# Kernel optimization log

Measured on AMD Instinct MI355X. Metric: run time of the kernel, lower is better.

The kernel has to match this reference:

```python
import jax, jax.numpy as jnp
import numpy as np

D, H, FF, E, K, B, S = 1024, 16, 4096, 8, 2, 2, 2048
EPS = 1e-5


def _layernorm(x, g, b):
    mu = x.mean(-1, keepdims=True)
    var = x.var(-1, keepdims=True)
    return (x - mu) * jax.lax.rsqrt(var + EPS) * g + b


def setup_inputs() -> dict:
    key = jax.random.key(0)
    ks = jax.random.split(key, 16)
    s = 0.02
    return {
        "x": jax.random.normal(ks[0], (B, S, D), dtype=jnp.float32),
        "in_proj_w": jax.random.normal(ks[1], (3 * D, D), dtype=jnp.float32) * s,
        "in_proj_b": jnp.zeros((3 * D,), jnp.float32),
        "out_proj_w": jax.random.normal(ks[2], (D, D), dtype=jnp.float32) * s,
        "out_proj_b": jnp.zeros((D,), jnp.float32),
        "ln1_g": jnp.ones((D,), jnp.float32),
        "ln1_b": jnp.zeros((D,), jnp.float32),
        "ln2_g": jnp.ones((D,), jnp.float32),
        "ln2_b": jnp.zeros((D,), jnp.float32),
        "gate_w": jax.random.normal(ks[3], (E, D), dtype=jnp.float32) * s,
        "gate_b": jnp.zeros((E,), jnp.float32),
        "w1": jax.random.normal(ks[4], (E, FF, D), dtype=jnp.float32) * s,
        "b1": jnp.zeros((E, FF), jnp.float32),
        "w2": jax.random.normal(ks[5], (E, D, FF), dtype=jnp.float32) * s,
        "b2": jnp.zeros((E, D), jnp.float32),
    }


def reference(x, in_proj_w, in_proj_b, out_proj_w, out_proj_b,
              ln1_g, ln1_b, ln2_g, ln2_b,
              gate_w, gate_b, w1, b1, w2, b2):
    b, s, d = x.shape
    hd = d // H
    # --- self-attention (pre-LN), dropout = identity (eval) ---
    normed = _layernorm(x, ln1_g, ln1_b)
    qkv = normed @ in_proj_w.T + in_proj_b            # [b,s,3d]
    q, k, v = jnp.split(qkv, 3, axis=-1)
    q = q.reshape(b, s, H, hd).transpose(0, 2, 1, 3)  # [b,h,s,hd]
    k = k.reshape(b, s, H, hd).transpose(0, 2, 1, 3)
    v = v.reshape(b, s, H, hd).transpose(0, 2, 1, 3)
    scores = jnp.einsum('bhqe,bhke->bhqk', q, k) / np.sqrt(hd)
    attn = jax.nn.softmax(scores, axis=-1)
    o = jnp.einsum('bhqk,bhke->bhqe', attn, v)
    o = o.transpose(0, 2, 1, 3).reshape(b, s, d)
    attn_out = o @ out_proj_w.T + out_proj_b
    x = x + attn_out
    present_kv = (normed, normed)
    # --- MoE FFN ---
    n2 = _layernorm(x, ln2_g, ln2_b)
    xf = n2.reshape(-1, d)                             # [T,d]
    T = xf.shape[0]
    logits = xf @ gate_w.T + gate_b                    # [T,E]
    probs = jax.nn.softmax(logits, axis=-1)
    top_v, top_i = jax.lax.top_k(probs, K)             # [T,K]
    top_v = top_v / top_v.sum(-1, keepdims=True)
    # combine weights per (token, expert); topk indices are unique per token
    cw = jnp.zeros((T, E), probs.dtype).at[jnp.arange(T)[:, None], top_i].add(top_v)
    # dense all-experts FFN (mathematically identical to masked gather/scatter)
    h = jnp.einsum('td,efd->etf', xf, w1) + b1[:, None, :]   # [E,T,FF]
    h = jax.nn.gelu(h, approximate=False)
    eo = jnp.einsum('etf,edf->etd', h, w2) + b2[:, None, :]  # [E,T,d]
    moe_out = jnp.einsum('te,etd->td', cw, eo)               # [T,d]
    out = x + moe_out.reshape(b, s, d)
    # --- load balance loss (Switch) ---
    top1 = jnp.argmax(probs, axis=-1)
    f = jnp.mean(jax.nn.one_hot(top1, E, dtype=probs.dtype), axis=0)
    P = probs.mean(axis=0)
    load_loss = 0.01 * E * jnp.sum(f * P)
    return out, load_loss, probs.reshape(b, s, E), present_kv[0]
```

## Files before the change

### kernel.cpp

```cpp
#include <hip/hip_runtime.h>
#include <math.h>

#define D_ 1024
#define H_ 16
#define HD_ 64
#define FF_ 4096
#define E_ 8
#define B_ 2
#define S_ 2048
#define T_ 4096
#define MAXROWS 9216
#define MAXTILES 72

typedef unsigned short u16;
typedef __attribute__((ext_vector_type(4))) float f32x4;
typedef __attribute__((ext_vector_type(8))) __bf16 bf16x8;
typedef __attribute__((ext_vector_type(8))) _Float16 f16x8;
typedef __attribute__((ext_vector_type(4))) unsigned short u16x4;

__device__ __forceinline__ u16 f2bf(float f){
  union { float f; unsigned u; } v; v.f = f;
  unsigned r = v.u + 0x7fffu + ((v.u >> 16) & 1u);
  return (u16)(r >> 16);
}
__device__ __forceinline__ float bf2f(u16 h){
  union { unsigned u; float f; } v; v.u = ((unsigned)h) << 16;
  return v.f;
}
__device__ __forceinline__ void glds16(const void* g, void* l){
  __builtin_amdgcn_global_load_lds((const __attribute__((address_space(1))) void*)g,
                                   (__attribute__((address_space(3))) void*)l, 16, 0, 0);
}
__device__ __forceinline__ bf16x8 ld8(const u16* p){
  return *reinterpret_cast<const bf16x8*>(p);
}
__device__ __forceinline__ f16x8 ldH8(const _Float16* p){
  return *reinterpret_cast<const f16x8*>(p);
}
__device__ __forceinline__ f32x4 mfma16(bf16x8 a, bf16x8 b, f32x4 c){
  return __builtin_amdgcn_mfma_f32_16x16x32_bf16(a, b, c, 0, 0, 0);
}
__device__ __forceinline__ f32x4 mfmaH(f16x8 a, f16x8 b, f32x4 c){
  return __builtin_amdgcn_mfma_f32_16x16x32_f16(a, b, c, 0, 0, 0);
}
__device__ __forceinline__ unsigned pk16(float a, float b){
  auto pk = __builtin_amdgcn_cvt_pkrtz(a, b);
  return __builtin_bit_cast(unsigned, pk);
}

__global__ void __launch_bounds__(256) split_hl_kernel(const float* __restrict__ in, u16* __restrict__ hi,
                                                       u16* __restrict__ lo, int n4){
  int i = blockIdx.x*blockDim.x + threadIdx.x;
  if (i >= n4) return;
  float4 v = reinterpret_cast<const float4*>(in)[i];
  float vv[4] = {v.x, v.y, v.z, v.w};
  u16x4 h, l;
  #pragma unroll
  for (int j=0;j<4;j++){
    u16 hh = f2bf(vv[j]);
    h[j] = hh;
    l[j] = f2bf(vv[j] - bf2f(hh));
  }
  reinterpret_cast<u16x4*>(hi)[i] = h;
  reinterpret_cast<u16x4*>(lo)[i] = l;
}

__global__ void __launch_bounds__(256) cvt_bf_kernel(const float* __restrict__ in, u16* __restrict__ out, int n4){
  int i = blockIdx.x*blockDim.x + threadIdx.x;
  if (i >= n4) return;
  float4 v = reinterpret_cast<const float4*>(in)[i];
  u16x4 o;
  o[0]=f2bf(v.x); o[1]=f2bf(v.y); o[2]=f2bf(v.z); o[3]=f2bf(v.w);
  reinterpret_cast<u16x4*>(out)[i] = o;
}

__global__ void __launch_bounds__(256) cvt_f16_kernel(const float* __restrict__ in, _Float16* __restrict__ out, int n4){
  int i = blockIdx.x*blockDim.x + threadIdx.x;
  if (i >= n4) return;
  float4 v = reinterpret_cast<const float4*>(in)[i];
  union { unsigned w[2]; u16x4 u; } o;
  o.w[0] = pk16(v.x, v.y);
  o.w[1] = pk16(v.z, v.w);
  reinterpret_cast<u16x4*>(out)[i] = o.u;
}

template<int OUTMODE>
__global__ void __launch_bounds__(256) ln_kernel(const float* __restrict__ x, const float* __restrict__ g,
    const float* __restrict__ bta, float* __restrict__ outf, u16* __restrict__ nout)
{
  const int t = blockIdx.x, tid = threadIdx.x;
  const float4 v = reinterpret_cast<const float4*>(x + (size_t)t*D_)[tid];
  float s  = v.x+v.y+v.z+v.w;
  float s2 = v.x*v.x+v.y*v.y+v.z*v.z+v.w*v.w;
  #pragma unroll
  for (int o=32;o;o>>=1){ s += __shfl_xor(s,o); s2 += __shfl_xor(s2,o); }
  __shared__ float rs[4], rq[4];
  const int wid=tid>>6, lane=tid&63;
  if (lane==0){ rs[wid]=s; rq[wid]=s2; }
  __syncthreads();
  s  = rs[0]+rs[1]+rs[2]+rs[3];
  s2 = rq[0]+rq[1]+rq[2]+rq[3];
  const float mu  = s*(1.0f/D_);
  const float var = s2*(1.0f/D_) - mu*mu;
  const float inv = rsqrtf(var + 1e-5f);
  const float4 gv = reinterpret_cast<const float4*>(g)[tid];
  const float4 bv = reinterpret_cast<const float4*>(bta)[tid];
  float oo[4];
  oo[0] = (v.x-mu)*inv*gv.x + bv.x;
  oo[1] = (v.y-mu)*inv*gv.y + bv.y;
  oo[2] = (v.z-mu)*inv*gv.z + bv.z;
  oo[3] = (v.w-mu)*inv*gv.w + bv.w;
  const size_t base = (size_t)t*D_ + tid*4;
  if (outf){ outf[base]=oo[0]; outf[base+1]=oo[1]; outf[base+2]=oo[2]; outf[base+3]=oo[3]; }
  if (OUTMODE==1){
    union { unsigned w[2]; u16x4 u; } hv;
    hv.w[0] = pk16(oo[0], oo[1]);
    hv.w[1] = pk16(oo[2], oo[3]);
    reinterpret_cast<u16x4*>(nout)[base>>2] = hv.u;
  } else {
    u16x4 hv;
    hv[0]=f2bf(oo[0]); hv[1]=f2bf(oo[1]); hv[2]=f2bf(oo[2]); hv[3]=f2bf(oo[3]);
    reinterpret_cast<u16x4*>(nout)[base>>2] = hv;
  }
}

__global__ void __launch_bounds__(256) qkv_kernel(
    const _Float16* __restrict__ A, const _Float16* __restrict__ Bw,
    const float* __restrict__ bias,
    _Float16* __restrict__ qf, _Float16* __restrict__ kf, _Float16* __restrict__ vtf)
{
  __shared__ __align__(16) _Float16 Ash[2][128*32], Bsh[2][128*32];
  const int bid = blockIdx.x, nwg = gridDim.x;
  const int fid = (bid & 7)*(nwg>>3) + (bid>>3);
  const int nt = fid % 24, mt = fid / 24;
  const int tid=threadIdx.x, wid=tid>>6, lane=tid&63;
  const int wr=wid>>1, wc=wid&1;
  const int r16=lane&15, g4=lane>>4;
  const _Float16* Ag = A  + (size_t)mt*128*D_;
  const _Float16* Bg = Bw + (size_t)nt*128*D_;
  const int srow = wid*16 + (lane>>2);
  const int scol = (((lane&3) ^ ((lane>>3)&3)))*8;
  const int sl   = (g4 ^ ((r16>>1)&3))*8;
  f32x4 acc[4][4] = {};
#define QSTAGE(bi, k0) do { \
    _Pragma("unroll") \
    for (int p=0;p<2;p++){ \
      const int r  = p*64 + srow; \
      const int lo = (p*64 + wid*16)*32; \
      glds16(Ag + (size_t)r*D_ + (k0) + scol, &Ash[bi][lo]); \
      glds16(Bg + (size_t)r*D_ + (k0) + scol, &Bsh[bi][lo]); \
    } \
  } while(0)
  QSTAGE(0, 0);
  int cur = 0;
  for (int t=0; t<D_/32; ++t){
    if (t+1 < D_/32){
      QSTAGE(cur^1, (t+1)*32);
      asm volatile("s_waitcnt vmcnt(4)" ::: "memory");
    } else {
      asm volatile("s_waitcnt vmcnt(0)" ::: "memory");
    }
    __syncthreads();
    f16x8 af[4], bfr[4];
    #pragma unroll
    for (int m=0;m<4;m++) af[m]=ldH8(&Ash[cur][(wr*64+m*16+r16)*32 + sl]);
    #pragma unroll
    for (int n=0;n<4;n++) bfr[n]=ldH8(&Bsh[cur][(wc*64+n*16+r16)*32 + sl]);
    #pragma unroll
    for (int m=0;m<4;m++){
      #pragma unroll
      for (int n=0;n<4;n++) acc[m][n] = mfmaH(af[m], bfr[n], acc[m][n]);
    }
    __syncthreads();
    cur ^= 1;
  }
#undef QSTAGE
  #pragma unroll
  for (int m=0;m<4;m++){
    #pragma unroll
    for (int n=0;n<4;n++){
      #pragma unroll
      for (int r=0;r<4;r++){
        const int grow = mt*128 + wr*64 + m*16 + g4*4 + r;
        const int gcol = nt*128 + wc*64 + n*16 + r16;
        const float val = acc[m][n][r] + bias[gcol];
        const int which = gcol>>10, rem = gcol&1023;
        const int hh = rem>>6, ee = rem&63;
        const int bb = grow>>11, ss = grow&2047;
        if (which==0){
          qf[((size_t)(bb*H_+hh)*S_ + ss)*HD_ + ee] = (_Float16)(val * 0.18033688f);
        } else if (which==1){
          kf[((size_t)(bb*H_+hh)*S_ + ss)*HD_ + ee] = (_Float16)val;
        } else {
          const int p32 = 2*(ss & 12) + (ss & 3) + 4*((ss >> 4) & 1);
          const size_t idx = (((size_t)(bb*H_+hh)*(S_/32) + (ss>>5))*HD_ + ee)*32 + p32;
          vtf[idx] = (_Float16)val;
        }
      }
    }
  }
}

__global__ void __launch_bounds__(256) gemm3_kernel(
    const u16* __restrict__ Ah, const u16* __restrict__ Al, int lda,
    const u16* __restrict__ Bh, const u16* __restrict__ Bl, int Kdim,
    const float* __restrict__ bias,
    const float* __restrict__ resid, float* __restrict__ x1out)
{
  __shared__ __align__(16) u16 Ash[2][128*32], Asl[2][128*32], Bsh[2][128*32], Bsl[2][128*32];
  const int bid = blockIdx.x, nwg = gridDim.x;
  const int fid = (bid & 7)*(nwg>>3) + (bid>>3);
  const int nt = fid & 7, mt = fid >> 3;
  const int tid=threadIdx.x, wid=tid>>6, lane=tid&63;
  const int wr=wid>>1, wc=wid&1;
  const int r16=lane&15, g4=lane>>4;
  const u16* Agh = Ah + (size_t)mt*128*lda;
  const u16* Agl = Al + (size_t)mt*128*lda;
  const u16* Bgh = Bh + (size_t)nt*128*Kdim;
  const u16* Bgl = Bl + (size_t)nt*128*Kdim;
  const int srow = wid*16 + (lane>>2);
  const int scol = (((lane&3) ^ ((lane>>3)&3)))*8;
  const int sl   = (g4 ^ ((r16>>1)&3))*8;
  f32x4 acc[4][4] = {};
#define G3STAGE(bi, k0) do { \
    _Pragma("unroll") \
    for (int p=0;p<2;p++){ \
      const int r  = p*64 + srow; \
      const int lo = (p*64 + wid*16)*32; \
      glds16(Agh + (size_t)r*lda  + (k0) + scol, &Ash[bi][lo]); \
      glds16(Agl + (size_t)r*lda  + (k0) + scol, &Asl[bi][lo]); \
      glds16(Bgh + (size_t)r*Kdim + (k0) + scol, &Bsh[bi][lo]); \
      glds16(Bgl + (size_t)r*Kdim + (k0) + scol, &Bsl[bi][lo]); \
    } \
  } while(0)
  G3STAGE(0, 0);
  int cur = 0;
  const int NK = Kdim/32;
  for (int t=0; t<NK; ++t){
    if (t+1 < NK){
      G3STAGE(cur^1, (t+1)*32);
      asm volatile("s_waitcnt vmcnt(8)" ::: "memory");
    } else {
      asm volatile("s_waitcnt vmcnt(0)" ::: "memory");
    }
    __syncthreads();
    bf16x8 afh[4], afl[4], bfh[4], bfl[4];
    #pragma unroll
    for (int m=0;m<4;m++){
      const int row = wr*64 + m*16 + r16;
      afh[m] = ld8(&Ash[cur][row*32 + sl]);
      afl[m] = ld8(&Asl[cur][row*32 + sl]);
    }
    #pragma unroll
    for (int n=0;n<4;n++){
      const int row = wc*64 + n*16 + r16;
      bfh[n] = ld8(&Bsh[cur][row*32 + sl]);
      bfl[n] = ld8(&Bsl[cur][row*32 + sl]);
    }
    #pragma unroll
    for (int m=0;m<4;m++){
      #pragma unroll
      for (int n=0;n<4;n++){
        acc[m][n] = mfma16(afl[m], bfh[n], acc[m][n]);
        acc[m][n] = mfma16(afh[m], bfl[n], acc[m][n]);
        acc[m][n] = mfma16(afh[m], bfh[n], acc[m][n]);
      }
    }
    __syncthreads();
    cur ^= 1;
  }
#undef G3STAGE
  #pragma unroll
  for (int m=0;m<4;m++){
    #pragma unroll
    for (int n=0;n<4;n++){
      #pragma unroll
      for (int r=0;r<4;r++){
        const int grow = mt*128 + wr*64 + m*16 + g4*4 + r;
        const int gcol = nt*128 + wc*64 + n*16 + r16;
        const float val = acc[m][n][r] + bias[gcol];
        const size_t idx = (size_t)grow*D_ + gcol;
        x1out[idx] = val + resid[idx];
      }
    }
  }
}

__global__ void __launch_bounds__(256) attn9_kernel(
    const _Float16* __restrict__ Qf, const _Float16* __restrict__ Kf,
    const _Float16* __restrict__ Vtf,
    u16* __restrict__ Oh, u16* __restrict__ Ol)
{
  __shared__ __align__(16) _Float16 Kb[2][4096];
  __shared__ __align__(16) _Float16 Vb[2][4096];
  const int bid = blockIdx.x;
  const int wg = (bid & 7) * 128 + (bid >> 3);
  const int bh = wg >> 5, qc = wg & 31;
  const int tid=threadIdx.x, wid=tid>>6, lane=tid&63;
  const int r16=lane&15, g4=lane>>4;
  const int q0 = qc*64 + wid*16;
  const _Float16* Qp = Qf  + (size_t)bh*S_*HD_ + (size_t)(q0+r16)*HD_ + g4*8;
  const _Float16* Kbase = Kf  + (size_t)bh*S_*HD_;
  const _Float16* Vbase = Vtf + (size_t)bh*HD_*S_;
  const f16x8 qf0 = ldH8(Qp);
  const f16x8 qf1 = ldH8(Qp+32);
  f32x4 of[4] = {};
  float m_run = -3e38f, lr = 0.f;

  const int kOff = (wid*8 + (lane>>3))*HD_ + (((lane&7) ^ ((lane>>3)&7)))*8;
  const int vOff = wid*512 + lane*8;
  const int sk0 = (g4 ^ (r16&7))*8;
  const int sk1 = ((g4+4) ^ (r16&7))*8;

#define STAGE(bi, tt) do { \
    glds16(Kbase + (size_t)(tt)*64*HD_ + kOff,          (void*)&Kb[bi][wid*512]); \
    glds16(Kbase + (size_t)(tt)*64*HD_ + 32*HD_ + kOff, (void*)&Kb[bi][2048 + wid*512]); \
    glds16(Vbase + (size_t)(tt)*4096 + vOff,            (void*)&Vb[bi][wid*512]); \
    glds16(Vbase + (size_t)(tt)*4096 + 2048 + vOff,     (void*)&Vb[bi][2048 + wid*512]); \
  } while(0)

#define ATT_HALF(Kh_, Vh_) do { \
    const f16x8 k0v = ldH8((Kh_) + r16*64 + sk0); \
    const f16x8 k1v = ldH8((Kh_) + r16*64 + sk1); \
    const f16x8 k2v = ldH8((Kh_) + (16+r16)*64 + sk0); \
    const f16x8 k3v = ldH8((Kh_) + (16+r16)*64 + sk1); \
    f32x4 sA={}, sB={}; \
    __builtin_amdgcn_s_setprio(1); \
    sA = mfmaH(k0v, qf0, sA); sA = mfmaH(k1v, qf1, sA); \
    sB = mfmaH(k2v, qf0, sB); sB = mfmaH(k3v, qf1, sB); \
    __builtin_amdgcn_s_setprio(0); \
    const float t0=sA[0], t1=sA[1], t2=sA[2], t3=sA[3]; \
    const float t4=sB[0], t5=sB[1], t6=sB[2], t7=sB[3]; \
    const float lmx = fmaxf(fmaxf(fmaxf(t0,t1),fmaxf(t2,t3)), \
                            fmaxf(fmaxf(t4,t5),fmaxf(t6,t7))); \
    if (!__all(lmx <= m_run + 4.0f)) { \
      float mx = fmaxf(lmx, __shfl_xor(lmx,16)); \
      mx = fmaxf(mx, __shfl_xor(mx,32)); \
      const float mn = fmaxf(m_run, mx); \
      const float alp = __builtin_amdgcn_exp2f(m_run - mn); \
      m_run = mn; \
      lr *= alp; \
      const float ao0=__shfl(alp,4*g4), ao1=__shfl(alp,4*g4+1); \
      const float ao2=__shfl(alp,4*g4+2), ao3=__shfl(alp,4*g4+3); \
      _Pragma("unroll") \
      for (int c=0;c<4;c++){ of[c][0]*=ao0; of[c][1]*=ao1; of[c][2]*=ao2; of[c][3]*=ao3; } \
    } \
    const float msh = m_run - 9.0f; \
    const float p0=__builtin_amdgcn_exp2f(t0-msh), p1=__builtin_amdgcn_exp2f(t1-msh); \
    const float p2=__builtin_amdgcn_exp2f(t2-msh), p3=__builtin_amdgcn_exp2f(t3-msh); \
    const float p4=__builtin_amdgcn_exp2f(t4-msh), p5=__builtin_amdgcn_exp2f(t5-msh); \
    const float p6=__builtin_amdgcn_exp2f(t6-msh), p7=__builtin_amdgcn_exp2f(t7-msh); \
    lr += ((p0+p1)+(p2+p3)) + ((p4+p5)+(p6+p7)); \
    union { unsigned w[4]; f16x8 v; } pu; \
    pu.w[0]=pk16(p0,p1); pu.w[1]=pk16(p2,p3); \
    pu.w[2]=pk16(p4,p5); pu.w[3]=pk16(p6,p7); \
    const f16x8 v0v = ldH8((Vh_) + (r16)*32 + g4*8); \
    const f16x8 v1v = ldH8((Vh_) + (16+r16)*32 + g4*8); \
    const f16x8 v2v = ldH8((Vh_) + (32+r16)*32 + g4*8); \
    const f16x8 v3v = ldH8((Vh_) + (48+r16)*32 + g4*8); \
    __builtin_amdgcn_s_setprio(1); \
    of[0] = mfmaH(pu.v, v0v, of[0]); of[1] = mfmaH(pu.v, v1v, of[1]); \
    of[2] = mfmaH(pu.v, v2v, of[2]); of[3] = mfmaH(pu.v, v3v, of[3]); \
    __builtin_amdgcn_s_setprio(0); \
  } while(0)

  STAGE(0, 0);
  int cur = 0;

  for (int t=0; t<32; ++t){
    if (t < 31){
      STAGE(cur^1, t+1);
      asm volatile("s_waitcnt vmcnt(4)" ::: "memory");
    } else {
      asm volatile("s_waitcnt vmcnt(0)" ::: "memory");
    }
    __syncthreads();
    ATT_HALF(&Kb[cur][0],    &Vb[cur][0]);
    ATT_HALF(&Kb[cur][2048], &Vb[cur][2048]);
    __syncthreads();
    cur ^= 1;
  }
#undef ATT_HALF
#undef STAGE

  lr += __shfl_xor(lr,16);
  lr += __shfl_xor(lr,32);
  float li[4];
  #pragma unroll
  for (int r=0;r<4;r++) li[r] = 1.0f / __shfl(lr, 4*g4+r);
  const int bb = bh>>4, hh = bh&15;
  #pragma unroll
  for (int c=0;c<4;c++){
    #pragma unroll
    for (int r=0;r<4;r++){
      const float val = of[c][r] * li[r];
      const int qq = q0 + 4*g4 + r;
      const size_t idx = ((size_t)(bb*S_+qq))*D_ + hh*HD_ + c*16 + r16;
      const u16 hi = f2bf(val);
      Oh[idx]=hi; Ol[idx]=f2bf(val-bf2f(hi));
    }
  }
}

__global__ void __launch_bounds__(64) gate_kernel(
    const float* __restrict__ x1, const float* __restrict__ g2, const float* __restrict__ b2v,
    const float* __restrict__ gw, const float* __restrict__ gb,
    float* __restrict__ probs_out, int* __restrict__ top_i, float* __restrict__ cw_w)
{
  const int t = blockIdx.x, lane = threadIdx.x;
  const float* row = x1 + (size_t)t*D_;
  float xv[16];
  float s=0.f, s2=0.f;
  #pragma unroll
  for (int j=0;j<4;j++){
    float4 v = reinterpret_cast<const float4*>(row)[lane*4+j];
    xv[j*4]=v.x; xv[j*4+1]=v.y; xv[j*4+2]=v.z; xv[j*4+3]=v.w;
    s += v.x+v.y+v.z+v.w; s2 += v.x*v.x+v.y*v.y+v.z*v.z+v.w*v.w;
  }
  #pragma unroll
  for (int o=32;o;o>>=1){ s+=__shfl_xor(s,o); s2+=__shfl_xor(s2,o); }
  const float mu=s*(1.f/D_), var=s2*(1.f/D_)-mu*mu, inv=rsqrtf(var+1e-5f);
  float nv[16];
  #pragma unroll
  for (int j=0;j<4;j++){
    float4 gv = reinterpret_cast<const float4*>(g2)[lane*4+j];
    float4 bv = reinterpret_cast<const float4*>(b2v)[lane*4+j];
    nv[j*4]  =(xv[j*4]  -mu)*inv*gv.x+bv.x;
    nv[j*4+1]=(xv[j*4+1]-mu)*inv*gv.y+bv.y;
    nv[j*4+2]=(xv[j*4+2]-mu)*inv*gv.z+bv.z;
    nv[j*4+3]=(xv[j*4+3]-mu)*inv*gv.w+bv.w;
  }
  float acc[E_] = {};
  #pragma unroll
  for (int e=0;e<E_;e++){
    const float* w = gw + (size_t)e*D_ + lane*16;
    #pragma unroll
    for (int j=0;j<4;j++){
      float4 wv = reinterpret_cast<const float4*>(w)[j];
      acc[e] += nv[j*4]*wv.x + nv[j*4+1]*wv.y + nv[j*4+2]*wv.z + nv[j*4+3]*wv.w;
    }
  }
  #pragma unroll
  for (int e=0;e<E_;e++){
    #pragma unroll
    for (int o=32;o;o>>=1) acc[e]+=__shfl_xor(acc[e],o);
  }
  float lg[E_], mx=-3e38f;
  #pragma unroll
  for (int e=0;e<E_;e++){ lg[e]=acc[e]+gb[e]; mx=fmaxf(mx,lg[e]); }
  float ex[E_], sm=0.f;
  #pragma unroll
  for (int e=0;e<E_;e++){ ex[e]=__expf(lg[e]-mx); sm+=ex[e]; }
  float p[E_];
  #pragma unroll
  for (int e=0;e<E_;e++) p[e]=ex[e]/sm;
  if (lane<E_) probs_out[(size_t)t*E_+lane]=p[lane];
  int i0=0; float l0=lg[0];
  #pragma unroll
  for (int e=1;e<E_;e++) if (lg[e]>l0){ l0=lg[e]; i0=e; }
  int i1=-1; float l1=-3e38f;
  #pragma unroll
  for (int e=0;e<E_;e++) if (e!=i0 && lg[e]>l1){ l1=lg[e]; i1=e; }
  if (lane==0){
    top_i[2*t]=i0; top_i[2*t+1]=i1;
    const float v0=p[i0], v1=p[i1];
    const float swt=v0+v1;
    cw_w[2*t]=v0/swt; cw_w[2*t+1]=v1/swt;
  }
}

__global__ void __launch_bounds__(512) scan_kernel(const int* __restrict__ top_i,
    int* __restrict__ goff, int* __restrict__ tile_expert,
    int* __restrict__ assign_token, int* __restrict__ pos_of)
{
  __shared__ int cnt[E_];
  __shared__ int off[E_+1];
  const int tid=threadIdx.x;
  if (tid<E_) cnt[tid]=0;
  __syncthreads();
  for (int t=tid;t<T_;t+=512){
    atomicAdd(&cnt[top_i[2*t]],1);
    atomicAdd(&cnt[top_i[2*t+1]],1);
  }
  __syncthreads();
  if (tid==0){
    off[0]=0;
    for (int e=0;e<E_;e++) off[e+1]=off[e]+((cnt[e]+127)&~127);
    for (int i=0;i<=E_;i++) goff[i]=off[i];
  }
  __syncthreads();
  if (tid<MAXTILES){
    const int r=tid*128; int e=-1;
    for (int j=0;j<E_;j++) if (r>=off[j] && r<off[j+1]) e=j;
    tile_expert[tid]=e;
  }
  const int lane=tid&63;
  const int e=tid>>6;
  int base=off[e];
  for (int c=0;c<T_/64;c++){
    const int t=c*64+lane;
    const int a0=top_i[2*t], a1=top_i[2*t+1];
    const bool f=(a0==e)||(a1==e);
    const unsigned long long m=__ballot(f);
    if (f){
      const int pos = base + (int)__popcll(m & ((1ull<<lane)-1ull));
      assign_token[pos]=t;
      pos_of[2*t + (a0==e?0:1)] = pos;
    }
    base += (int)__popcll(m);
  }
  for (int r=base+lane; r<off[e+1]; r+=64) assign_token[r]=-1;
  __syncthreads();
  for (int r=off[E_]+tid; r<MAXROWS; r+=512) assign_token[r]=-1;
}

__global__ void __launch_bounds__(256) gather_kernel(const int* __restrict__ assign_token,
    const u16* __restrict__ n2b, u16* __restrict__ xg)
{
  const int r = blockIdx.x;
  const int t = assign_token[r];
  u16x4 val = {};
  if (t>=0) val = reinterpret_cast<const u16x4*>(n2b + (size_t)t*D_)[threadIdx.x];
  reinterpret_cast<u16x4*>(xg + (size_t)r*D_)[threadIdx.x] = val;
}

template<int MODE>
__global__ void __launch_bounds__(256, 4) gemm_grp_kernel(
    const u16* __restrict__ A, int lda,
    const u16* __restrict__ Bbase, int Kdim, int Nsz, int NT,
    const float* __restrict__ bias,
    const int* __restrict__ tile_expert,
    u16* __restrict__ outp)
{
  const int bid = blockIdx.x, nwg = gridDim.x;
  const int fid = (bid & 7)*(nwg>>3) + (bid>>3);
  const int nt = fid % NT, mt = fid / NT;
  const int e = tile_expert[mt];
  if (e<0) return;
  __shared__ __align__(16) u16 Ash[2][128*32], Bsh[2][128*32];
  const int tid=threadIdx.x, wid=tid>>6, lane=tid&63;
  const int wr=wid>>1, wc=wid&1;
  const int r16=lane&15, g4=lane>>4;
  const u16* Ag = A + (size_t)mt*128*lda;
  const u16* Bg = Bbase + (size_t)e*Nsz*Kdim + (size_t)nt*128*Kdim;
  const float* bp = bias + (size_t)e*Nsz;
  const int srow = wid*16 + (lane>>2);
  const int scol = (((lane&3) ^ ((lane>>3)&3)))*8;
  const int sl   = (g4 ^ ((r16>>1)&3))*8;
  f32x4 acc[4][4] = {};
#define GSTAGE(bi, k0) do { \
    _Pragma("unroll") \
    for (int p=0;p<2;p++){ \
      const int r  = p*64+srow; \
      const int lo = (p*64+wid*16)*32; \
      glds16(Ag + (size_t)r*lda  + (k0) + scol, &Ash[bi][lo]); \
      glds16(Bg + (size_t)r*Kdim + (k0) + scol, &Bsh[bi][lo]); \
    } \
  } while(0)
  GSTAGE(0, 0);
  int cur = 0;
  const int NK = Kdim/32;
  for (int t=0; t<NK; ++t){
    if (t+1 < NK){
      GSTAGE(cur^1, (t+1)*32);
      asm volatile("s_waitcnt vmcnt(4)" ::: "memory");
    } else {
      asm volatile("s_waitcnt vmcnt(0)" ::: "memory");
    }
    __syncthreads();
    bf16x8 af[4], bfr[4];
    #pragma unroll
    for (int m=0;m<4;m++) af[m]=ld8(&Ash[cur][(wr*64+m*16+r16)*32 + sl]);
    #pragma unroll
    for (int n=0;n<4;n++) bfr[n]=ld8(&Bsh[cur][(wc*64+n*16+r16)*32 + sl]);
    #pragma unroll
    for (int m=0;m<4;m++){
      #pragma unroll
      for (int n=0;n<4;n++) acc[m][n] = mfma16(af[m], bfr[n], acc[m][n]);
    }
    __syncthreads();
    cur ^= 1;
  }
#undef GSTAGE
  #pragma unroll
  for (int m=0;m<4;m++){
    #pragma unroll
    for (int n=0;n<4;n++){
      #pragma unroll
      for (int r=0;r<4;r++){
        const int grow = mt*128 + wr*64 + m*16 + g4*4 + r;
        const int gcol = nt*128 + wc*64 + n*16 + r16;
        float val = acc[m][n][r] + bp[gcol];
        if (MODE==2){
          const float z = val*(1.0f + 0.044715f*val*val)*2.3021622f;
          val = val / (1.0f + __builtin_amdgcn_exp2f(-z));
        }
        outp[(size_t)grow*Nsz + gcol] = f2bf(val);
      }
    }
  }
}

__global__ void __launch_bounds__(256) combine_kernel(const float* __restrict__ x1,
    const u16* __restrict__ eo, const int* __restrict__ pos_of, const float* __restrict__ cw_w,
    float* __restrict__ out0)
{
  const int t=blockIdx.x, tid=threadIdx.x;
  const int r0=pos_of[2*t], r1=pos_of[2*t+1];
  const float w0=cw_w[2*t], w1=cw_w[2*t+1];
  const u16x4 e0 = reinterpret_cast<const u16x4*>(eo + (size_t)r0*D_)[tid];
  const u16x4 e1 = reinterpret_cast<const u16x4*>(eo + (size_t)r1*D_)[tid];
  const float4 xv = reinterpret_cast<const float4*>(x1 + (size_t)t*D_)[tid];
  float4 o;
  o.x = xv.x + w0*bf2f(e0[0]) + w1*bf2f(e1[0]);
  o.y = xv.y + w0*bf2f(e0[1]) + w1*bf2f(e1[1]);
  o.z = xv.z + w0*bf2f(e0[2]) + w1*bf2f(e1[2]);
  o.w = xv.w + w0*bf2f(e0[3]) + w1*bf2f(e1[3]);
  reinterpret_cast<float4*>(out0 + (size_t)t*D_)[tid] = o;
}

__global__ void __launch_bounds__(256) loss_kernel(const float* __restrict__ probs,
    const int* __restrict__ top_i, float* __restrict__ loss_out)
{
  const int tid=threadIdx.x;
  float f[E_]={0,0,0,0,0,0,0,0}, P[E_]={0,0,0,0,0,0,0,0};
  for (int t=tid;t<T_;t+=256){
    const float* pr = probs + (size_t)t*E_;
    const int a0 = top_i[2*t];
    #pragma unroll
    for (int e=0;e<E_;e++){
      P[e] += pr[e];
      f[e] += (a0==e) ? 1.0f : 0.0f;
    }
  }
  #pragma unroll
  for (int e=0;e<E_;e++){
    #pragma unroll
    for (int o=32;o;o>>=1){ f[e]+=__shfl_xor(f[e],o); P[e]+=__shfl_xor(P[e],o); }
  }
  __shared__ float sf[4][E_], sP[4][E_];
  const int wid=tid>>6, lane=tid&63;
  if (lane==0){
    #pragma unroll
    for (int e=0;e<E_;e++){ sf[wid][e]=f[e]; sP[wid][e]=P[e]; }
  }
  __syncthreads();
  if (tid==0){
    float loss=0.f;
    #pragma unroll
    for (int e=0;e<E_;e++){
      const float fe=sf[0][e]+sf[1][e]+sf[2][e]+sf[3][e];
      const float Pe=sP[0][e]+sP[1][e]+sP[2][e]+sP[3][e];
      loss += (fe/(float)T_)*(Pe/(float)T_);
    }
    loss_out[0] = 0.01f*(float)E_*loss;
  }
}

static inline size_t alup(size_t x){ return (x+255)&~(size_t)255; }

extern "C" void kernel_launch(void* const* d_in, const int* in_sizes, int n_in,
                              void* d_out, int out_size, void* d_ws, size_t ws_size,
                              hipStream_t stream) {
  (void)in_sizes; (void)n_in; (void)out_size; (void)ws_size;
  const float* x    = (const float*)d_in[0];
  const float* ipw  = (const float*)d_in[1];
  const float* ipb  = (const float*)d_in[2];
  const float* opw  = (const float*)d_in[3];
  const float* opb  = (const float*)d_in[4];
  const float* ln1g = (const float*)d_in[5];
  const float* ln1b = (const float*)d_in[6];
  const float* ln2g = (const float*)d_in[7];
  const float* ln2b = (const float*)d_in[8];
  const float* gw   = (const float*)d_in[9];
  const float* gb   = (const float*)d_in[10];
  const float* w1   = (const float*)d_in[11];
  const float* b1   = (const float*)d_in[12];
  const float* w2   = (const float*)d_in[13];
  const float* b2   = (const float*)d_in[14];

  float* out0       = (float*)d_out;
  float* loss_out   = out0 + (size_t)T_*D_;
  float* probs_out  = loss_out + 1;
  float* normed_out = probs_out + (size_t)T_*E_;

  char* p = (char*)d_ws;
  auto take = [&](size_t bytes)->void*{ void* r = (void*)p; p += alup(bytes); return r; };

  _Float16* wipf = (_Float16*)take((size_t)3*D_*D_*2);
  u16* wop_h = (u16*)take((size_t)D_*D_*2);
  u16* wop_l = (u16*)take((size_t)D_*D_*2);
  u16* w1b   = (u16*)take((size_t)E_*FF_*D_*2);
  u16* w2b   = (u16*)take((size_t)E_*D_*FF_*2);
  _Float16* nf16 = (_Float16*)take((size_t)T_*D_*2);
  _Float16* qf  = (_Float16*)take((size_t)T_*D_*2);
  _Float16* kf  = (_Float16*)take((size_t)T_*D_*2);
  _Float16* vtf = (_Float16*)take((size_t)T_*D_*2);
  u16* oh    = (u16*)take((size_t)T_*D_*2);
  u16* ol    = (u16*)take((size_t)T_*D_*2);
  float* x1  = (float*)take((size_t)T_*D_*4);
  u16* n2b   = (u16*)take((size_t)T_*D_*2);
  u16* xg    = (u16*)take((size_t)MAXROWS*D_*2);
  u16* hbuf  = (u16*)take((size_t)MAXROWS*FF_*2);
  u16* eo    = (u16*)take((size_t)MAXROWS*D_*2);
  int* top_i = (int*)take((size_t)T_*2*4);
  float* cww = (float*)take((size_t)T_*2*4);
  int* posof = (int*)take((size_t)T_*2*4);
  int* goff  = (int*)take((size_t)(E_+1)*4);
  int* texp  = (int*)take((size_t)MAXTILES*4);
  int* atok  = (int*)take((size_t)MAXROWS*4);

  cvt_f16_kernel<<<(3*D_*D_/4+255)/256, 256, 0, stream>>>(ipw, wipf, 3*D_*D_/4);
  split_hl_kernel<<<(D_*D_/4+255)/256, 256, 0, stream>>>(opw, wop_h, wop_l, D_*D_/4);
  cvt_bf_kernel<<<(E_*FF_*D_/4+255)/256, 256, 0, stream>>>(w1, w1b, E_*FF_*D_/4);
  cvt_bf_kernel<<<(E_*D_*FF_/4+255)/256, 256, 0, stream>>>(w2, w2b, E_*D_*FF_/4);

  ln_kernel<1><<<T_, 256, 0, stream>>>(x, ln1g, ln1b, normed_out, (u16*)nf16);

  qkv_kernel<<<dim3(24*(T_/128)), 256, 0, stream>>>(nf16, wipf, ipb, qf, kf, vtf);

  attn9_kernel<<<B_*H_*(S_/64), 256, 0, stream>>>(qf, kf, vtf, oh, ol);

  gemm3_kernel<<<dim3(8*(T_/128)), 256, 0, stream>>>(
      oh, ol, D_, wop_h, wop_l, D_, opb, x, x1);

  ln_kernel<2><<<T_, 256, 0, stream>>>(x1, ln2g, ln2b, nullptr, n2b);

  gate_kernel<<<T_, 64, 0, stream>>>(x1, ln2g, ln2b, gw, gb, probs_out, top_i, cww);

  scan_kernel<<<1, 512, 0, stream>>>(top_i, goff, texp, atok, posof);

  gather_kernel<<<MAXROWS, 256, 0, stream>>>(atok, n2b, xg);

  gemm_grp_kernel<2><<<dim3((FF_/128)*MAXTILES), 256, 0, stream>>>(xg, D_, w1b, D_, FF_, FF_/128, b1, texp, hbuf);
  gemm_grp_kernel<3><<<dim3((D_/128)*MAXTILES), 256, 0, stream>>>(hbuf, FF_, w2b, FF_, D_, D_/128, b2, texp, eo);

  combine_kernel<<<T_, 256, 0, stream>>>(x1, eo, posof, cww, out0);
  loss_kernel<<<1, 256, 0, stream>>>(probs_out, top_i, loss_out);
}
```

Measured before the change: 545.9 us.

## Convert expert weights to bf16 inside grouped GEMM and fuse gate into LN2

Drops the two standalone fp32-to-bf16 conversion kernels for the expert weights. The grouped GEMM now loads fp32 weight tiles into registers, converts them and writes them into swizzled LDS, with the global loads issued before the MFMAs and the LDS writes after them. Occupancy is lowered to 3 waves per SIMD. Separately, the router gate (logits, softmax, top-2) is fused into the second LayerNorm kernel so x1 is read once. The cost is more global bytes for the B operand per tile, repeated across token tiles, plus conversion ALU work inside the GEMM inner loop.

```diff
diff --git a/kernel.cpp b/kernel.cpp
--- a/kernel.cpp
+++ b/kernel.cpp
@@ -26,6 +26,9 @@
 __device__ __forceinline__ float bf2f(u16 h){
   union { unsigned u; float f; } v; v.u = ((unsigned)h) << 16;
   return v.f;
+}
+__device__ __forceinline__ unsigned pb2(float a, float b){
+  return (unsigned)f2bf(a) | ((unsigned)f2bf(b) << 16);
 }
 __device__ __forceinline__ void glds16(const void* g, void* l){
   __builtin_amdgcn_global_load_lds((const __attribute__((address_space(1))) void*)g,
@@ -65,15 +68,6 @@
   reinterpret_cast<u16x4*>(lo)[i] = l;
 }
 
-__global__ void __launch_bounds__(256) cvt_bf_kernel(const float* __restrict__ in, u16* __restrict__ out, int n4){
-  int i = blockIdx.x*blockDim.x + threadIdx.x;
-  if (i >= n4) return;
-  float4 v = reinterpret_cast<const float4*>(in)[i];
-  u16x4 o;
-  o[0]=f2bf(v.x); o[1]=f2bf(v.y); o[2]=f2bf(v.z); o[3]=f2bf(v.w);
-  reinterpret_cast<u16x4*>(out)[i] = o;
-}
-
 __global__ void __launch_bounds__(256) cvt_f16_kernel(const float* __restrict__ in, _Float16* __restrict__ out, int n4){
   int i = blockIdx.x*blockDim.x + threadIdx.x;
   if (i >= n4) return;
@@ -84,17 +78,20 @@
   reinterpret_cast<u16x4*>(out)[i] = o.u;
 }
 
-template<int OUTMODE>
+template<int OUTMODE, int GATE>
 __global__ void __launch_bounds__(256) ln_kernel(const float* __restrict__ x, const float* __restrict__ g,
-    const float* __restrict__ bta, float* __restrict__ outf, u16* __restrict__ nout)
+    const float* __restrict__ bta, float* __restrict__ outf, u16* __restrict__ nout,
+    const float* __restrict__ gw, const float* __restrict__ gb,
+    float* __restrict__ probs_out, int* __restrict__ top_i, float* __restrict__ cw_w)
 {
   const int t = blockIdx.x, tid = threadIdx.x;
+  __shared__ float rs[4], rq[4];
+  __shared__ float sp[4][E_];
   const float4 v = reinterpret_cast<const float4*>(x + (size_t)t*D_)[tid];
   float s  = v.x+v.y+v.z+v.w;
   float s2 = v.x*v.x+v.y*v.y+v.z*v.z+v.w*v.w;
   #pragma unroll
   for (int o=32;o;o>>=1){ s += __shfl_xor(s,o); s2 += __shfl_xor(s2,o); }
-  __shared__ float rs[4], rq[4];
   const int wid=tid>>6, lane=tid&63;
   if (lane==0){ rs[wid]=s; rq[wid]=s2; }
   __syncthreads();
@@ -121,6 +118,48 @@
     u16x4 hv;
     hv[0]=f2bf(oo[0]); hv[1]=f2bf(oo[1]); hv[2]=f2bf(oo[2]); hv[3]=f2bf(oo[3]);
     reinterpret_cast<u16x4*>(nout)[base>>2] = hv;
+  }
+  if (GATE){
+    float part[E_];
+    #pragma unroll
+    for (int e=0;e<E_;e++){
+      const float4 wv = reinterpret_cast<const float4*>(gw + (size_t)e*D_)[tid];
+      part[e] = oo[0]*wv.x + oo[1]*wv.y + oo[2]*wv.z + oo[3]*wv.w;
+    }
+    #pragma unroll
+    for (int e=0;e<E_;e++){
+      #pragma unroll
+      for (int o=32;o;o>>=1) part[e] += __shfl_xor(part[e], o);
+    }
+    if (lane==0){
+      #pragma unroll
+      for (int e=0;e<E_;e++) sp[wid][e] = part[e];
+    }
+    __syncthreads();
+    if (tid==0){
+      float lg[E_], mx=-3e38f;
+      #pragma unroll
+      for (int e=0;e<E_;e++){
+        lg[e] = sp[0][e]+sp[1][e]+sp[2][e]+sp[3][e] + gb[e];
+        mx = fmaxf(mx, lg[e]);
+      }
+      float ex[E_], sm=0.f;
+      #pragma unroll
+      for (int e=0;e<E_;e++){ ex[e]=__expf(lg[e]-mx); sm+=ex[e]; }
+      float p[E_];
+      #pragma unroll
+      for (int e=0;e<E_;e++){ p[e]=ex[e]/sm; probs_out[(size_t)t*E_+e]=p[e]; }
+      int i0=0; float l0=lg[0];
+      #pragma unroll
+      for (int e=1;e<E_;e++) if (lg[e]>l0){ l0=lg[e]; i0=e; }
+      int i1=-1; float l1=-3e38f;
+      #pragma unroll
+      for (int e=0;e<E_;e++) if (e!=i0 && lg[e]>l1){ l1=lg[e]; i1=e; }
+      top_i[2*t]=i0; top_i[2*t+1]=i1;
+      const float v0=p[i0], v1=p[i1];
+      const float swt=v0+v1;
+      cw_w[2*t]=v0/swt; cw_w[2*t+1]=v1/swt;
+    }
   }
 }
 
@@ -402,73 +441,6 @@
   }
 }
 
-__global__ void __launch_bounds__(64) gate_kernel(
-    const float* __restrict__ x1, const float* __restrict__ g2, const float* __restrict__ b2v,
-    const float* __restrict__ gw, const float* __restrict__ gb,
-    float* __restrict__ probs_out, int* __restrict__ top_i, float* __restrict__ cw_w)
-{
-  const int t = blockIdx.x, lane = threadIdx.x;
-  const float* row = x1 + (size_t)t*D_;
-  float xv[16];
-  float s=0.f, s2=0.f;
-  #pragma unroll
-  for (int j=0;j<4;j++){
-    float4 v = reinterpret_cast<const float4*>(row)[lane*4+j];
-    xv[j*4]=v.x; xv[j*4+1]=v.y; xv[j*4+2]=v.z; xv[j*4+3]=v.w;
-    s += v.x+v.y+v.z+v.w; s2 += v.x*v.x+v.y*v.y+v.z*v.z+v.w*v.w;
-  }
-  #pragma unroll
-  for (int o=32;o;o>>=1){ s+=__shfl_xor(s,o); s2+=__shfl_xor(s2,o); }
-  const float mu=s*(1.f/D_), var=s2*(1.f/D_)-mu*mu, inv=rsqrtf(var+1e-5f);
-  float nv[16];
-  #pragma unroll
-  for (int j=0;j<4;j++){
-    float4 gv = reinterpret_cast<const float4*>(g2)[lane*4+j];
-    float4 bv = reinterpret_cast<const float4*>(b2v)[lane*4+j];
-    nv[j*4]  =(xv[j*4]  -mu)*inv*gv.x+bv.x;
-    nv[j*4+1]=(xv[j*4+1]-mu)*inv*gv.y+bv.y;
-    nv[j*4+2]=(xv[j*4+2]-mu)*inv*gv.z+bv.z;
-    nv[j*4+3]=(xv[j*4+3]-mu)*inv*gv.w+bv.w;
-  }
-  float acc[E_] = {};
-  #pragma unroll
-  for (int e=0;e<E_;e++){
-    const float* w = gw + (size_t)e*D_ + lane*16;
-    #pragma unroll
-    for (int j=0;j<4;j++){
-      float4 wv = reinterpret_cast<const float4*>(w)[j];
-      acc[e] += nv[j*4]*wv.x + nv[j*4+1]*wv.y + nv[j*4+2]*wv.z + nv[j*4+3]*wv.w;
-    }
-  }
-  #pragma unroll
-  for (int e=0;e<E_;e++){
-    #pragma unroll
-    for (int o=32;o;o>>=1) acc[e]+=__shfl_xor(acc[e],o);
-  }
-  float lg[E_], mx=-3e38f;
-  #pragma unroll
-  for (int e=0;e<E_;e++){ lg[e]=acc[e]+gb[e]; mx=fmaxf(mx,lg[e]); }
-  float ex[E_], sm=0.f;
-  #pragma unroll
-  for (int e=0;e<E_;e++){ ex[e]=__expf(lg[e]-mx); sm+=ex[e]; }
-  float p[E_];
-  #pragma unroll
-  for (int e=0;e<E_;e++) p[e]=ex[e]/sm;
-  if (lane<E_) probs_out[(size_t)t*E_+lane]=p[lane];
-  int i0=0; float l0=lg[0];
-  #pragma unroll
-  for (int e=1;e<E_;e++) if (lg[e]>l0){ l0=lg[e]; i0=e; }
-  int i1=-1; float l1=-3e38f;
-  #pragma unroll
-  for (int e=0;e<E_;e++) if (e!=i0 && lg[e]>l1){ l1=lg[e]; i1=e; }
-  if (lane==0){
-    top_i[2*t]=i0; top_i[2*t+1]=i1;
-    const float v0=p[i0], v1=p[i1];
-    const float swt=v0+v1;
-    cw_w[2*t]=v0/swt; cw_w[2*t+1]=v1/swt;
-  }
-}
-
 __global__ void __launch_bounds__(512) scan_kernel(const int* __restrict__ top_i,
     int* __restrict__ goff, int* __restrict__ tile_expert,
     int* __restrict__ assign_token, int* __restrict__ pos_of)
@@ -525,9 +497,9 @@
 }
 
 template<int MODE>
-__global__ void __launch_bounds__(256, 4) gemm_grp_kernel(
+__global__ void __launch_bounds__(256, 3) gemm_grp_kernel(
     const u16* __restrict__ A, int lda,
-    const u16* __restrict__ Bbase, int Kdim, int Nsz, int NT,
+    const float* __restrict__ B32, int Kdim, int Nsz, int NT,
     const float* __restrict__ bias,
     const int* __restrict__ tile_expert,
     u16* __restrict__ outp)
@@ -541,33 +513,53 @@
   const int tid=threadIdx.x, wid=tid>>6, lane=tid&63;
   const int wr=wid>>1, wc=wid&1;
   const int r16=lane&15, g4=lane>>4;
-  const u16* Ag = A + (size_t)mt*128*lda;
-  const u16* Bg = Bbase + (size_t)e*Nsz*Kdim + (size_t)nt*128*Kdim;
+  const u16*   Ag   = A   + (size_t)mt*128*lda;
+  const float* Bg32 = B32 + (size_t)e*Nsz*Kdim + (size_t)nt*128*Kdim;
   const float* bp = bias + (size_t)e*Nsz;
   const int srow = wid*16 + (lane>>2);
   const int scol = (((lane&3) ^ ((lane>>3)&3)))*8;
   const int sl   = (g4 ^ ((r16>>1)&3))*8;
+  const int br = tid>>2, bg = tid&3;
+  const int bslot = (bg ^ ((br>>1)&3))*8;
+  float4 bv0, bv1, bv2, bv3;
   f32x4 acc[4][4] = {};
-#define GSTAGE(bi, k0) do { \
+#define ASTAGE(bi, k0) do { \
     _Pragma("unroll") \
     for (int p=0;p<2;p++){ \
       const int r  = p*64+srow; \
       const int lo = (p*64+wid*16)*32; \
-      glds16(Ag + (size_t)r*lda  + (k0) + scol, &Ash[bi][lo]); \
-      glds16(Bg + (size_t)r*Kdim + (k0) + scol, &Bsh[bi][lo]); \
+      glds16(Ag + (size_t)r*lda + (k0) + scol, &Ash[bi][lo]); \
     } \
   } while(0)
-  GSTAGE(0, 0);
+#define BLOAD(k0) do { \
+    const float* bp0 = Bg32 + (size_t)br*Kdim + (k0) + bg*8; \
+    const float* bp1 = Bg32 + (size_t)(br+64)*Kdim + (k0) + bg*8; \
+    bv0 = *reinterpret_cast<const float4*>(bp0); \
+    bv1 = *reinterpret_cast<const float4*>(bp0+4); \
+    bv2 = *reinterpret_cast<const float4*>(bp1); \
+    bv3 = *reinterpret_cast<const float4*>(bp1+4); \
+  } while(0)
+#define BWRITE(bi) do { \
+    uint4 w0, w1; \
+    w0.x = pb2(bv0.x,bv0.y); w0.y = pb2(bv0.z,bv0.w); \
+    w0.z = pb2(bv1.x,bv1.y); w0.w = pb2(bv1.z,bv1.w); \
+    w1.x = pb2(bv2.x,bv2.y); w1.y = pb2(bv2.z,bv2.w); \
+    w1.z = pb2(bv3.x,bv3.y); w1.w = pb2(bv3.z,bv3.w); \
+    *reinterpret_cast<uint4*>(&Bsh[bi][br*32 + bslot]) = w0; \
+    *reinterpret_cast<uint4*>(&Bsh[bi][(br+64)*32 + bslot]) = w1; \
+  } while(0)
+  BLOAD(0);
+  ASTAGE(0, 0);
+  BWRITE(0);
+  asm volatile("s_waitcnt vmcnt(0)" ::: "memory");
+  __syncthreads();
   int cur = 0;
   const int NK = Kdim/32;
   for (int t=0; t<NK; ++t){
     if (t+1 < NK){
-      GSTAGE(cur^1, (t+1)*32);
-      asm volatile("s_waitcnt vmcnt(4)" ::: "memory");
-    } else {
-      asm volatile("s_waitcnt vmcnt(0)" ::: "memory");
-    }
-    __syncthreads();
+      BLOAD((t+1)*32);
+      ASTAGE(cur^1, (t+1)*32);
+    }
     bf16x8 af[4], bfr[4];
     #pragma unroll
     for (int m=0;m<4;m++) af[m]=ld8(&Ash[cur][(wr*64+m*16+r16)*32 + sl]);
@@ -578,10 +570,14 @@
       #pragma unroll
       for (int n=0;n<4;n++) acc[m][n] = mfma16(af[m], bfr[n], acc[m][n]);
     }
+    if (t+1 < NK) BWRITE(cur^1);
+    asm volatile("s_waitcnt vmcnt(0)" ::: "memory");
     __syncthreads();
     cur ^= 1;
   }
-#undef GSTAGE
+#undef BWRITE
+#undef BLOAD
+#undef ASTAGE
   #pragma unroll
   for (int m=0;m<4;m++){
     #pragma unroll
@@ -690,8 +686,6 @@
   _Float16* wipf = (_Float16*)take((size_t)3*D_*D_*2);
   u16* wop_h = (u16*)take((size_t)D_*D_*2);
   u16* wop_l = (u16*)take((size_t)D_*D_*2);
-  u16* w1b   = (u16*)take((size_t)E_*FF_*D_*2);
-  u16* w2b   = (u16*)take((size_t)E_*D_*FF_*2);
   _Float16* nf16 = (_Float16*)take((size_t)T_*D_*2);
   _Float16* qf  = (_Float16*)take((size_t)T_*D_*2);
   _Float16* kf  = (_Float16*)take((size_t)T_*D_*2);
@@ -712,10 +706,9 @@
 
   cvt_f16_kernel<<<(3*D_*D_/4+255)/256, 256, 0, stream>>>(ipw, wipf, 3*D_*D_/4);
   split_hl_kernel<<<(D_*D_/4+255)/256, 256, 0, stream>>>(opw, wop_h, wop_l, D_*D_/4);
-  cvt_bf_kernel<<<(E_*FF_*D_/4+255)/256, 256, 0, stream>>>(w1, w1b, E_*FF_*D_/4);
-  cvt_bf_kernel<<<(E_*D_*FF_/4+255)/256, 256, 0, stream>>>(w2, w2b, E_*D_*FF_/4);
-
-  ln_kernel<1><<<T_, 256, 0, stream>>>(x, ln1g, ln1b, normed_out, (u16*)nf16);
+
+  ln_kernel<1,0><<<T_, 256, 0, stream>>>(x, ln1g, ln1b, normed_out, (u16*)nf16,
+                                         nullptr, nullptr, nullptr, nullptr, nullptr);
 
   qkv_kernel<<<dim3(24*(T_/128)), 256, 0, stream>>>(nf16, wipf, ipb, qf, kf, vtf);
 
@@ -724,16 +717,15 @@
   gemm3_kernel<<<dim3(8*(T_/128)), 256, 0, stream>>>(
       oh, ol, D_, wop_h, wop_l, D_, opb, x, x1);
 
-  ln_kernel<2><<<T_, 256, 0, stream>>>(x1, ln2g, ln2b, nullptr, n2b);
-
-  gate_kernel<<<T_, 64, 0, stream>>>(x1, ln2g, ln2b, gw, gb, probs_out, top_i, cww);
+  ln_kernel<2,1><<<T_, 256, 0, stream>>>(x1, ln2g, ln2b, nullptr, n2b,
+                                         gw, gb, probs_out, top_i, cww);
 
   scan_kernel<<<1, 512, 0, stream>>>(top_i, goff, texp, atok, posof);
 
   gather_kernel<<<MAXROWS, 256, 0, stream>>>(atok, n2b, xg);
 
-  gemm_grp_kernel<2><<<dim3((FF_/128)*MAXTILES), 256, 0, stream>>>(xg, D_, w1b, D_, FF_, FF_/128, b1, texp, hbuf);
-  gemm_grp_kernel<3><<<dim3((D_/128)*MAXTILES), 256, 0, stream>>>(hbuf, FF_, w2b, FF_, D_, D_/128, b2, texp, eo);
+  gemm_grp_kernel<2><<<dim3((FF_/128)*MAXTILES), 256, 0, stream>>>(xg, D_, w1, D_, FF_, FF_/128, b1, texp, hbuf);
+  gemm_grp_kernel<3><<<dim3((D_/128)*MAXTILES), 256, 0, stream>>>(hbuf, FF_, w2, FF_, D_, D_/128, b2, texp, eo);
 
   combine_kernel<<<T_, 256, 0, stream>>>(x1, eo, posof, cww, out0);
   loss_kernel<<<1, 256, 0, stream>>>(probs_out, top_i, loss_out);
```

Result: slower. 602.7 us (+10.4%).
